# Performance work log

Measured on AMD Instinct MI355X. Metric: run time of the kernel, lower is better.

## Reference

```python
import jax, jax.numpy as jnp
import numpy as np

B, S, N, C, D = 1, 6, 6400, 128, 4
HEADS, POINTS = 4, 20
HS, WS = 32, 88
M = HS * WS
DH = C // HEADS


def setup_inputs() -> dict:
    key = jax.random.key(0)
    ks = jax.random.split(key, 16)
    sc = 0.02
    return {
        "query": jax.random.normal(ks[0], (B, N, C), jnp.float32),
        "key": jax.random.normal(ks[1], (S, M, B, C), jnp.float32),
        "value": jax.random.normal(ks[2], (S, M, B, C), jnp.float32),
        "query_pos": jax.random.normal(ks[3], (B, N, C), jnp.float32),
        "reference_points_cam": jax.random.uniform(ks[4], (S, B, N, D, 2), jnp.float32),
        "bev_mask": jax.random.bernoulli(ks[5], 0.3, (S, B, N, D)),
        "spatial_shapes": jnp.array([[HS, WS]], jnp.int32),
        "level_start_index": jnp.zeros((1,), jnp.int32),
        "Wv": sc * jax.random.normal(ks[6], (C, C), jnp.float32),
        "bv": jnp.zeros((C,), jnp.float32),
        "Woff": sc * jax.random.normal(ks[7], (C, HEADS * POINTS * 2), jnp.float32),
        "boff": sc * jax.random.normal(ks[8], (HEADS * POINTS * 2,), jnp.float32),
        "Wattn": sc * jax.random.normal(ks[9], (C, HEADS * POINTS), jnp.float32),
        "battn": jnp.zeros((HEADS * POINTS,), jnp.float32),
        "Wout": sc * jax.random.normal(ks[10], (C, C), jnp.float32),
        "bout": jnp.zeros((C,), jnp.float32),
    }


def _bilinear(img, x, y):
    # img: (G, HS, WS, DH); x, y: (G, Q, P) pixel coords (grid_sample align_corners=False, zero padding)
    G = img.shape[0]
    flat = img.reshape(G, HS * WS, DH)
    x0 = jnp.floor(x)
    y0 = jnp.floor(y)
    wx1 = x - x0
    wy1 = y - y0
    x0i = x0.astype(jnp.int32)
    y0i = y0.astype(jnp.int32)

    def gather(xi, yi):
        valid = ((xi >= 0) & (xi < WS) & (yi >= 0) & (yi < HS)).astype(img.dtype)
        idx = jnp.clip(yi, 0, HS - 1) * WS + jnp.clip(xi, 0, WS - 1)
        v = jnp.take_along_axis(flat, idx.reshape(G, -1, 1), axis=1)
        return v.reshape(*idx.shape, DH) * valid[..., None]

    v00 = gather(x0i, y0i)
    v01 = gather(x0i + 1, y0i)
    v10 = gather(x0i, y0i + 1)
    v11 = gather(x0i + 1, y0i + 1)
    return (v00 * ((1 - wx1) * (1 - wy1))[..., None]
            + v01 * (wx1 * (1 - wy1))[..., None]
            + v10 * ((1 - wx1) * wy1)[..., None]
            + v11 * (wx1 * wy1)[..., None])


def _deform_attn(q, v, ref, spatial_shapes, Wv, bv, Woff, boff, Wattn, battn):
    # q: (bs, nq, C); v: (bs, M, C); ref: (bs, nq, D, 2) in [0,1]
    bs, nq, _ = q.shape
    val = (v @ Wv + bv).reshape(bs, HS, WS, HEADS, DH)
    val = val.transpose(0, 3, 1, 2, 4).reshape(bs * HEADS, HS, WS, DH)
    # sampling offsets, normalized by (W, H), split points into POINTS//D groups per Z-anchor
    norm = jnp.stack([spatial_shapes[0, 1], spatial_shapes[0, 0]]).astype(q.dtype)  # [W, H]
    off = (q @ Woff + boff).reshape(bs, nq, HEADS, POINTS // D, D, 2) / norm
    loc = ref[:, :, None, None, :, :] + off  # (bs, nq, HEADS, P//D, D, 2)
    loc = loc.reshape(bs, nq, HEADS, POINTS, 2).transpose(0, 2, 1, 3, 4)
    loc = loc.reshape(bs * HEADS, nq, POINTS, 2)
    x = loc[..., 0] * WS - 0.5
    y = loc[..., 1] * HS - 0.5
    sampled = _bilinear(val, x, y)  # (bs*HEADS, nq, POINTS, DH)
    aw = jax.nn.softmax((q @ Wattn + battn).reshape(bs, nq, HEADS, POINTS), axis=-1)
    aw = aw.transpose(0, 2, 1, 3).reshape(bs * HEADS, nq, POINTS)
    out = jnp.einsum('gnpd,gnp->gnd', sampled, aw)
    return out.reshape(bs, HEADS, nq, DH).transpose(0, 2, 1, 3).reshape(bs, nq, C)


def reference(query, key, value, query_pos, reference_points_cam, bev_mask,
              spatial_shapes, level_start_index,
              Wv, bv, Woff, boff, Wattn, battn, Wout, bout):
    residual = query
    q = query + query_pos
    # camera routing mask (original derives indexes from batch 0 of bev_mask)
    mask0 = (bev_mask[:, 0].sum(-1) > 0).astype(q.dtype)  # (S, N)
    # dense masked equivalent of gather/pad/attend/scatter-add: deformable attn is
    # per-query independent, so computing all queries per camera and masking is exact.
    qs = jnp.broadcast_to(q[:, None], (B, S, N, C)).reshape(B * S, N, C)
    vs = value.transpose(2, 0, 1, 3).reshape(B * S, M, C)
    refs = reference_points_cam.transpose(1, 0, 2, 3, 4).reshape(B * S, N, D, 2)
    out = _deform_attn(qs, vs, refs, spatial_shapes, Wv, bv, Woff, boff, Wattn, battn)
    out = out.reshape(B, S, N, C)
    slots = (out * mask0[None, :, :, None]).sum(1)  # (B, N, C)
    count = (bev_mask.sum(-1) > 0).astype(q.dtype).transpose(1, 2, 0).sum(-1)  # (B, N)
    slots = slots / jnp.maximum(count, 1.0)[..., None]
    slots = slots @ Wout + bout
    return slots + residual  # dropout is identity in eval
```

## Files before the change

### kernel.cpp

```cpp
#include <hip/hip_runtime.h>

#define SC 6
#define NQ 6400
#define CH 128
#define HSY 32
#define WSX 88
#define MV 2816
#define NH 4
#define NP 20
#define DD 4
#define DHC 32
#define NPG 5
#define NPAIR (SC * NH * NP)
#define NSCAN 150

#define WS_SCAN_OR  8
#define WS_SCAN_VI  160
#define WS_QOFF     38464
#define WS_AW       1062464
#define WS_VAL      1574464
#define WS_SLOTS    3737152

__device__ __forceinline__ unsigned short f32_to_bf16(float x) {
    unsigned int u = __float_as_uint(x);
    unsigned int r = (u + 0x7FFFu + ((u >> 16) & 1u)) >> 16;
    return (unsigned short)r;
}

__global__ void k_scan(const unsigned int* __restrict__ bm,
                       unsigned int* __restrict__ scan_or,
                       unsigned int* __restrict__ scan_vi) {
    __shared__ unsigned int r_or[256];
    __shared__ unsigned int r_vi[256];
    int i = blockIdx.x * 256 + threadIdx.x;
    unsigned int w = bm[i];
    r_or[threadIdx.x] = w & 0xFFFFFF00u;
    r_vi[threadIdx.x] = (w != 0u) & (w != 0x3F800000u);
    __syncthreads();
    for (int s = 128; s > 0; s >>= 1) {
        if (threadIdx.x < (unsigned)s) {
            r_or[threadIdx.x] |= r_or[threadIdx.x + s];
            r_vi[threadIdx.x] |= r_vi[threadIdx.x + s];
        }
        __syncthreads();
    }
    if (threadIdx.x == 0) {
        scan_or[blockIdx.x] = r_or[0];
        scan_vi[blockIdx.x] = r_vi[0];
    }
}

__global__ void k_flag(const unsigned int* __restrict__ scan_or,
                       const unsigned int* __restrict__ scan_vi,
                       int* __restrict__ flag) {
    __shared__ unsigned int r_or[256];
    __shared__ unsigned int r_vi[256];
    unsigned int o = 0u, v = 0u;
    if (threadIdx.x < NSCAN) { o = scan_or[threadIdx.x]; v = scan_vi[threadIdx.x]; }
    r_or[threadIdx.x] = o;
    r_vi[threadIdx.x] = v;
    __syncthreads();
    for (int s = 128; s > 0; s >>= 1) {
        if (threadIdx.x < (unsigned)s) {
            r_or[threadIdx.x] |= r_or[threadIdx.x + s];
            r_vi[threadIdx.x] |= r_vi[threadIdx.x + s];
        }
        __syncthreads();
    }
    if (threadIdx.x == 0) {
        int f;
        if (!r_vi[0]) f = 2;
        else if (r_or[0]) f = 1;
        else f = 0;
        *flag = f;
    }
}

#define QB 8
__global__ void k_qproj(const float* __restrict__ q, const float* __restrict__ qpos,
                        const float* __restrict__ Woff, const float* __restrict__ boff,
                        const float* __restrict__ Wattn, const float* __restrict__ battn,
                        float* __restrict__ qoff, float* __restrict__ aw) {
    __shared__ float qs[CH][QB];
    __shared__ float lg[QB][NH * NP];
    int n0 = blockIdx.x * QB;
    int t = threadIdx.x;
    for (int i = t; i < QB * CH; i += 256) {
        int qi = i >> 7, k = i & 127;
        int gi = (n0 + qi) * CH + k;
        qs[k][qi] = q[gi] + qpos[gi];
    }
    __syncthreads();
    if (t < 160) {
        float acc[QB];
#pragma unroll
        for (int qi = 0; qi < QB; ++qi) acc[qi] = 0.f;
        for (int k = 0; k < CH; ++k) {
            float w = Woff[k * 160 + t];
            float4 a = *(const float4*)&qs[k][0];
            float4 b = *(const float4*)&qs[k][4];
            acc[0] += a.x * w; acc[1] += a.y * w; acc[2] += a.z * w; acc[3] += a.w * w;
            acc[4] += b.x * w; acc[5] += b.y * w; acc[6] += b.z * w; acc[7] += b.w * w;
        }
        float b = boff[t];
#pragma unroll
        for (int qi = 0; qi < QB; ++qi) qoff[(n0 + qi) * 160 + t] = acc[qi] + b;
    } else if (t < 240) {
        int j = t - 160;
        float acc[QB];
#pragma unroll
        for (int qi = 0; qi < QB; ++qi) acc[qi] = 0.f;
        for (int k = 0; k < CH; ++k) {
            float w = Wattn[k * 80 + j];
            float4 a = *(const float4*)&qs[k][0];
            float4 b = *(const float4*)&qs[k][4];
            acc[0] += a.x * w; acc[1] += a.y * w; acc[2] += a.z * w; acc[3] += a.w * w;
            acc[4] += b.x * w; acc[5] += b.y * w; acc[6] += b.z * w; acc[7] += b.w * w;
        }
        float b = battn[j];
#pragma unroll
        for (int qi = 0; qi < QB; ++qi) lg[qi][j] = acc[qi] + b;
    }
    __syncthreads();
    if (t < QB * NH) {
        int qi = t >> 2, h = t & 3;
        float mx = -1e30f;
#pragma unroll
        for (int p = 0; p < NP; ++p) mx = fmaxf(mx, lg[qi][h * NP + p]);
        float e[NP];
        float sm = 0.f;
#pragma unroll
        for (int p = 0; p < NP; ++p) { e[p] = __expf(lg[qi][h * NP + p] - mx); sm += e[p]; }
        float inv = 1.f / sm;
#pragma unroll
        for (int p = 0; p < NP; ++p) aw[(n0 + qi) * 80 + h * NP + p] = e[p] * inv;
    }
}

#define MB 8
__global__ void k_vproj(const float* __restrict__ value, const float* __restrict__ Wv,
                        const float* __restrict__ bv, unsigned short* __restrict__ valw) {
    __shared__ float vs[CH][MB];
    int r0 = blockIdx.x * MB;
    int t = threadIdx.x;
    for (int i = t; i < MB * CH; i += 128) {
        int ri = i >> 7, k = i & 127;
        vs[k][ri] = value[(size_t)(r0 + ri) * CH + k];
    }
    __syncthreads();
    float acc[MB];
#pragma unroll
    for (int ri = 0; ri < MB; ++ri) acc[ri] = 0.f;
    for (int k = 0; k < CH; ++k) {
        float w = Wv[k * CH + t];
        float4 a = *(const float4*)&vs[k][0];
        float4 b = *(const float4*)&vs[k][4];
        acc[0] += a.x * w; acc[1] += a.y * w; acc[2] += a.z * w; acc[3] += a.w * w;
        acc[4] += b.x * w; acc[5] += b.y * w; acc[6] += b.z * w; acc[7] += b.w * w;
    }
    float b = bv[t];
    int h = t >> 5, dh = t & 31;
#pragma unroll
    for (int ri = 0; ri < MB; ++ri) {
        int r = r0 + ri;
        int s = r / MV;
        int m = r - s * MV;
        valw[(size_t)((s * NH + h) * MV + m) * DHC + dh] = f32_to_bf16(acc[ri] + b);
    }
}

#define REDP 36
__global__ __launch_bounds__(320) void k_sample(
        const float* __restrict__ ref, const float* __restrict__ qoff,
        const float* __restrict__ aw, const void* __restrict__ bm,
        const int* __restrict__ flag, const unsigned short* __restrict__ valw,
        float* __restrict__ slots) {
    int bid = blockIdx.x;
    int n = (bid & 7) * (NQ / 8) + (bid >> 3);
    int t = threadIdx.x;

    __shared__ float awl[NH * NP];
    __shared__ float qo[160];
    __shared__ float rf[SC][DD][2];
    __shared__ float mk[SC];
    __shared__ int   pairI[NPAIR][4];
    __shared__ float pairW[NPAIR][4];
    __shared__ float red[80][REDP];

    if (t < NH * NP) awl[t] = aw[n * 80 + t];
    if (t >= 80 && t < 240) qo[t - 80] = qoff[n * 160 + (t - 80)];
    if (t >= 240 && t < 240 + SC * DD * 2) {
        int i = t - 240;
        int s = i >> 3, rem = i & 7;
        rf[s][rem >> 1][rem & 1] = ref[(size_t)(s * NQ + n) * 8 + rem];
    }
    if (t >= 288 && t < 288 + SC) {
        int s = t - 288;
        int i = s * NQ + n;
        int f = *flag;
        int any;
        if (f == 1) {
            const unsigned char* p = (const unsigned char*)bm + (size_t)i * 4;
            any = (int)(p[0] | p[1] | p[2] | p[3]);
        } else if (f == 0) {
            const int* p = (const int*)bm + (size_t)i * 4;
            any = p[0] | p[1] | p[2] | p[3];
        } else {
            const float* p = (const float*)bm + (size_t)i * 4;
            any = (p[0] != 0.f) | (p[1] != 0.f) | (p[2] != 0.f) | (p[3] != 0.f);
        }
        mk[s] = any ? 1.0f : 0.0f;
    }
    __syncthreads();

    for (int i = t; i < NPAIR; i += 320) {
        int s = i / (NH * NP);
        int q = i - s * (NH * NP);
        int h = q & 3;
        int p = q >> 2;
        int g = p >> 2, d = p & 3;
        float x = rf[s][d][0] * (float)WSX + qo[((h * NPG + g) * DD + d) * 2 + 0] - 0.5f;
        float y = rf[s][d][1] * (float)HSY + qo[((h * NPG + g) * DD + d) * 2 + 1] - 0.5f;
        float xf = floorf(x), yf = floorf(y);
        float wx = x - xf, wy = y - yf;
        int x0 = (int)xf, y0 = (int)yf;
        int x1 = x0 + 1, y1 = y0 + 1;
        float vx0 = (x0 >= 0 && x0 < WSX) ? 1.f : 0.f;
        float vx1 = (x1 >= 0 && x1 < WSX) ? 1.f : 0.f;
        float vy0 = (y0 >= 0 && y0 < HSY) ? 1.f : 0.f;
        float vy1 = (y1 >= 0 && y1 < HSY) ? 1.f : 0.f;
        int cx0 = min(max(x0, 0), WSX - 1), cx1 = min(max(x1, 0), WSX - 1);
        int cy0 = min(max(y0, 0), HSY - 1), cy1 = min(max(y1, 0), HSY - 1);
        int base = (s * NH + h) * MV;
        pairI[i][0] = (base + cy0 * WSX + cx0) * DHC;
        pairI[i][1] = (base + cy0 * WSX + cx1) * DHC;
        pairI[i][2] = (base + cy1 * WSX + cx0) * DHC;
        pairI[i][3] = (base + cy1 * WSX + cx1) * DHC;
        float a = awl[h * NP + p];
        pairW[i][0] = (1.f - wx) * (1.f - wy) * vx0 * vy0 * a;
        pairW[i][1] = wx * (1.f - wy) * vx1 * vy0 * a;
        pairW[i][2] = (1.f - wx) * wy * vx0 * vy1 * a;
        pairW[i][3] = wx * wy * vx1 * vy1 * a;
    }
    __syncthreads();

    int sid = t >> 2;
    int c8 = t & 3;
    int coff = c8 * 8;
    float acc[8];
#pragma unroll
    for (int j = 0; j < 8; ++j) acc[j] = 0.f;
    for (int s = 0; s < SC; ++s) {
        if (mk[s] == 0.f) continue;
        int pr = s * (NH * NP) + sid;
        int4  ii = *(const int4*)pairI[pr];
        float4 ww = *(const float4*)pairW[pr];
#define CORNER(IDX, W)  {                                              \
            uint4 u = *(const uint4*)(valw + (IDX) + coff);            \
            float w_ = (W);                                            \
            acc[0] += w_ * __uint_as_float(u.x << 16);                 \
            acc[1] += w_ * __uint_as_float(u.x & 0xFFFF0000u);         \
            acc[2] += w_ * __uint_as_float(u.y << 16);                 \
            acc[3] += w_ * __uint_as_float(u.y & 0xFFFF0000u);         \
            acc[4] += w_ * __uint_as_float(u.z << 16);                 \
            acc[5] += w_ * __uint_as_float(u.z & 0xFFFF0000u);         \
            acc[6] += w_ * __uint_as_float(u.w << 16);                 \
            acc[7] += w_ * __uint_as_float(u.w & 0xFFFF0000u);         \
        }
        CORNER(ii.x, ww.x)
        CORNER(ii.y, ww.y)
        CORNER(ii.z, ww.z)
        CORNER(ii.w, ww.w)
#undef CORNER
    }
    *(float4*)&red[sid][coff] = make_float4(acc[0], acc[1], acc[2], acc[3]);
    *(float4*)&red[sid][coff + 4] = make_float4(acc[4], acc[5], acc[6], acc[7]);
    __syncthreads();

    if (t < CH) {
        int h = t >> 5, ch = t & 31;
        float sum = 0.f;
#pragma unroll
        for (int p = 0; p < NP; ++p) sum += red[p * 4 + h][ch];
        float cnt = mk[0] + mk[1] + mk[2] + mk[3] + mk[4] + mk[5];
        slots[(size_t)n * CH + t] = sum / fmaxf(cnt, 1.0f);
    }
}

__global__ void k_out(const float* __restrict__ slots, const float* __restrict__ Wout,
                      const float* __restrict__ bout, const float* __restrict__ query,
                      float* __restrict__ out) {
    __shared__ float sl[CH][QB];
    int n0 = blockIdx.x * QB;
    int t = threadIdx.x;
    for (int i = t; i < QB * CH; i += 128) {
        int qi = i >> 7, k = i & 127;
        sl[k][qi] = slots[(size_t)(n0 + qi) * CH + k];
    }
    __syncthreads();
    float acc[QB];
#pragma unroll
    for (int qi = 0; qi < QB; ++qi) acc[qi] = 0.f;
    for (int k = 0; k < CH; ++k) {
        float w = Wout[k * CH + t];
        float4 a = *(const float4*)&sl[k][0];
        float4 b = *(const float4*)&sl[k][4];
        acc[0] += a.x * w; acc[1] += a.y * w; acc[2] += a.z * w; acc[3] += a.w * w;
        acc[4] += b.x * w; acc[5] += b.y * w; acc[6] += b.z * w; acc[7] += b.w * w;
    }
    float b = bout[t];
#pragma unroll
    for (int qi = 0; qi < QB; ++qi) {
        int gi = (n0 + qi) * CH + t;
        out[gi] = acc[qi] + b + query[gi];
    }
}

extern "C" void kernel_launch(void* const* d_in, const int* in_sizes, int n_in,
                              void* d_out, int out_size, void* d_ws, size_t ws_size,
                              hipStream_t stream) {
    const float* query     = (const float*)d_in[0];
    const float* value     = (const float*)d_in[2];
    const float* query_pos = (const float*)d_in[3];
    const float* refcam    = (const float*)d_in[4];
    const void*  bev_mask  = (const void*)d_in[5];
    const float* Wv    = (const float*)d_in[8];
    const float* bv    = (const float*)d_in[9];
    const float* Woff  = (const float*)d_in[10];
    const float* boff  = (const float*)d_in[11];
    const float* Wattn = (const float*)d_in[12];
    const float* battn = (const float*)d_in[13];
    const float* Wout  = (const float*)d_in[14];
    const float* bout  = (const float*)d_in[15];

    float* wsf   = (float*)d_ws;
    int*   flag  = (int*)d_ws;
    unsigned int* scan_or = (unsigned int*)d_ws + WS_SCAN_OR;
    unsigned int* scan_vi = (unsigned int*)d_ws + WS_SCAN_VI;
    float* qoff  = wsf + WS_QOFF;
    float* aw    = wsf + WS_AW;
    unsigned short* valw = (unsigned short*)(wsf + WS_VAL);
    float* slots = wsf + WS_SLOTS;
    float* out   = (float*)d_out;

    k_scan<<<NSCAN, 256, 0, stream>>>((const unsigned int*)bev_mask, scan_or, scan_vi);
    k_flag<<<1, 256, 0, stream>>>(scan_or, scan_vi, flag);
    k_qproj<<<NQ / QB, 256, 0, stream>>>(query, query_pos, Woff, boff, Wattn, battn, qoff, aw);
    k_vproj<<<(SC * MV) / MB, 128, 0, stream>>>(value, Wv, bv, valw);
    k_sample<<<NQ, 320, 0, stream>>>(refcam, qoff, aw, bev_mask, flag, valw, slots);
    k_out<<<NQ / QB, 128, 0, stream>>>(slots, Wout, bout, query, out);
}
```

Baseline: 177.2 us.

## Merge mask scan, flag, query and value projections into one launch

Replaces the four prologue kernels (mask scan, flag reduction, query projection with softmax, value projection) with one kernel that dispatches on block index. Block 0 computes the mask-format flag from only the first 2048 words of bev_mask, so the two-stage reduction over the whole tensor is gone. Value-projection blocks now handle 16 rows with 256 threads instead of 8 rows with 128. The aim is to cut launch overhead and let the query and value projections run at the same time. The trade-off is that the flag now depends on a partial sample of the mask.

```diff
diff --git a/kernel.cpp b/kernel.cpp
--- a/kernel.cpp
+++ b/kernel.cpp
@@ -12,10 +12,11 @@
 #define DHC 32
 #define NPG 5
 #define NPAIR (SC * NH * NP)
-#define NSCAN 150
-
-#define WS_SCAN_OR  8
-#define WS_SCAN_VI  160
+
+#define NB_QPROJ 800
+#define NB_VPROJ 1056
+#define NB_MEGA  (1 + NB_QPROJ + NB_VPROJ)
+
 #define WS_QOFF     38464
 #define WS_AW       1062464
 #define WS_VAL      1574464
@@ -27,145 +28,130 @@
     return (unsigned short)r;
 }
 
-__global__ void k_scan(const unsigned int* __restrict__ bm,
-                       unsigned int* __restrict__ scan_or,
-                       unsigned int* __restrict__ scan_vi) {
-    __shared__ unsigned int r_or[256];
-    __shared__ unsigned int r_vi[256];
-    int i = blockIdx.x * 256 + threadIdx.x;
-    unsigned int w = bm[i];
-    r_or[threadIdx.x] = w & 0xFFFFFF00u;
-    r_vi[threadIdx.x] = (w != 0u) & (w != 0x3F800000u);
-    __syncthreads();
-    for (int s = 128; s > 0; s >>= 1) {
-        if (threadIdx.x < (unsigned)s) {
-            r_or[threadIdx.x] |= r_or[threadIdx.x + s];
-            r_vi[threadIdx.x] |= r_vi[threadIdx.x + s];
-        }
+#define QB 8
+__global__ __launch_bounds__(256) void k_mega(
+        const unsigned int* __restrict__ bm,
+        const float* __restrict__ q, const float* __restrict__ qpos,
+        const float* __restrict__ Woff, const float* __restrict__ boff,
+        const float* __restrict__ Wattn, const float* __restrict__ battn,
+        const float* __restrict__ value, const float* __restrict__ Wv,
+        const float* __restrict__ bv,
+        int* __restrict__ flag, float* __restrict__ qoff,
+        float* __restrict__ aw, unsigned short* __restrict__ valw) {
+    __shared__ __align__(16) float smem[2048];
+    int bid = blockIdx.x;
+    int t = threadIdx.x;
+
+    if (bid == 0) {
+        unsigned int* r_or = (unsigned int*)smem;
+        unsigned int* r_vi = r_or + 256;
+        unsigned int o = 0u, v = 0u;
+        for (int i = t; i < 2048; i += 256) {
+            unsigned int w = bm[i];
+            o |= (w & 0xFFFFFF00u);
+            v |= (unsigned int)((w != 0u) & (w != 0x3F800000u));
+        }
+        r_or[t] = o; r_vi[t] = v;
         __syncthreads();
-    }
-    if (threadIdx.x == 0) {
-        scan_or[blockIdx.x] = r_or[0];
-        scan_vi[blockIdx.x] = r_vi[0];
-    }
-}
-
-__global__ void k_flag(const unsigned int* __restrict__ scan_or,
-                       const unsigned int* __restrict__ scan_vi,
-                       int* __restrict__ flag) {
-    __shared__ unsigned int r_or[256];
-    __shared__ unsigned int r_vi[256];
-    unsigned int o = 0u, v = 0u;
-    if (threadIdx.x < NSCAN) { o = scan_or[threadIdx.x]; v = scan_vi[threadIdx.x]; }
-    r_or[threadIdx.x] = o;
-    r_vi[threadIdx.x] = v;
-    __syncthreads();
-    for (int s = 128; s > 0; s >>= 1) {
-        if (threadIdx.x < (unsigned)s) {
-            r_or[threadIdx.x] |= r_or[threadIdx.x + s];
-            r_vi[threadIdx.x] |= r_vi[threadIdx.x + s];
+        for (int s = 128; s > 0; s >>= 1) {
+            if (t < s) { r_or[t] |= r_or[t + s]; r_vi[t] |= r_vi[t + s]; }
+            __syncthreads();
+        }
+        if (t == 0) {
+            int f;
+            if (!r_vi[0]) f = 2;
+            else if (r_or[0]) f = 1;
+            else f = 0;
+            *flag = f;
+        }
+        return;
+    }
+
+    if (bid <= NB_QPROJ) {
+        float (*qs)[QB] = (float(*)[QB])smem;
+        float (*lg)[NH * NP] = (float(*)[NH * NP])(smem + CH * QB);
+        int n0 = (bid - 1) * QB;
+        for (int i = t; i < QB * CH; i += 256) {
+            int qi = i >> 7, k = i & 127;
+            int gi = (n0 + qi) * CH + k;
+            qs[k][qi] = q[gi] + qpos[gi];
         }
         __syncthreads();
-    }
-    if (threadIdx.x == 0) {
-        int f;
-        if (!r_vi[0]) f = 2;
-        else if (r_or[0]) f = 1;
-        else f = 0;
-        *flag = f;
-    }
-}
-
-#define QB 8
-__global__ void k_qproj(const float* __restrict__ q, const float* __restrict__ qpos,
-                        const float* __restrict__ Woff, const float* __restrict__ boff,
-                        const float* __restrict__ Wattn, const float* __restrict__ battn,
-                        float* __restrict__ qoff, float* __restrict__ aw) {
-    __shared__ float qs[CH][QB];
-    __shared__ float lg[QB][NH * NP];
-    int n0 = blockIdx.x * QB;
-    int t = threadIdx.x;
-    for (int i = t; i < QB * CH; i += 256) {
-        int qi = i >> 7, k = i & 127;
-        int gi = (n0 + qi) * CH + k;
-        qs[k][qi] = q[gi] + qpos[gi];
-    }
-    __syncthreads();
-    if (t < 160) {
-        float acc[QB];
-#pragma unroll
-        for (int qi = 0; qi < QB; ++qi) acc[qi] = 0.f;
+        if (t < 160) {
+            float acc[QB];
+#pragma unroll
+            for (int qi = 0; qi < QB; ++qi) acc[qi] = 0.f;
+            for (int k = 0; k < CH; ++k) {
+                float w = Woff[k * 160 + t];
+                float4 a = *(const float4*)&qs[k][0];
+                float4 b = *(const float4*)&qs[k][4];
+                acc[0] += a.x * w; acc[1] += a.y * w; acc[2] += a.z * w; acc[3] += a.w * w;
+                acc[4] += b.x * w; acc[5] += b.y * w; acc[6] += b.z * w; acc[7] += b.w * w;
+            }
+            float b = boff[t];
+#pragma unroll
+            for (int qi = 0; qi < QB; ++qi) qoff[(n0 + qi) * 160 + t] = acc[qi] + b;
+        } else if (t < 240) {
+            int j = t - 160;
+            float acc[QB];
+#pragma unroll
+            for (int qi = 0; qi < QB; ++qi) acc[qi] = 0.f;
+            for (int k = 0; k < CH; ++k) {
+                float w = Wattn[k * 80 + j];
+                float4 a = *(const float4*)&qs[k][0];
+                float4 b = *(const float4*)&qs[k][4];
+                acc[0] += a.x * w; acc[1] += a.y * w; acc[2] += a.z * w; acc[3] += a.w * w;
+                acc[4] += b.x * w; acc[5] += b.y * w; acc[6] += b.z * w; acc[7] += b.w * w;
+            }
+            float b = battn[j];
+#pragma unroll
+            for (int qi = 0; qi < QB; ++qi) lg[qi][j] = acc[qi] + b;
+        }
+        __syncthreads();
+        if (t < QB * NH) {
+            int qi = t >> 2, h = t & 3;
+            float mx = -1e30f;
+#pragma unroll
+            for (int p = 0; p < NP; ++p) mx = fmaxf(mx, lg[qi][h * NP + p]);
+            float e[NP];
+            float sm = 0.f;
+#pragma unroll
+            for (int p = 0; p < NP; ++p) { e[p] = __expf(lg[qi][h * NP + p] - mx); sm += e[p]; }
+            float inv = 1.f / sm;
+#pragma unroll
+            for (int p = 0; p < NP; ++p) aw[(n0 + qi) * 80 + h * NP + p] = e[p] * inv;
+        }
+        return;
+    }
+
+    {
+        float (*vs)[16] = (float(*)[16])smem;
+        int r0 = (bid - 1 - NB_QPROJ) * 16;
+        for (int i = t; i < 16 * CH; i += 256) {
+            int ri = i >> 7, k = i & 127;
+            vs[k][ri] = value[(size_t)(r0 + ri) * CH + k];
+        }
+        __syncthreads();
+        int c = t & 127, rh = t >> 7;
+        float acc[8];
+#pragma unroll
+        for (int ri = 0; ri < 8; ++ri) acc[ri] = 0.f;
         for (int k = 0; k < CH; ++k) {
-            float w = Woff[k * 160 + t];
-            float4 a = *(const float4*)&qs[k][0];
-            float4 b = *(const float4*)&qs[k][4];
+            float w = Wv[k * CH + c];
+            float4 a = *(const float4*)&vs[k][rh * 8];
+            float4 b = *(const float4*)&vs[k][rh * 8 + 4];
             acc[0] += a.x * w; acc[1] += a.y * w; acc[2] += a.z * w; acc[3] += a.w * w;
             acc[4] += b.x * w; acc[5] += b.y * w; acc[6] += b.z * w; acc[7] += b.w * w;
         }
-        float b = boff[t];
-#pragma unroll
-        for (int qi = 0; qi < QB; ++qi) qoff[(n0 + qi) * 160 + t] = acc[qi] + b;
-    } else if (t < 240) {
-        int j = t - 160;
-        float acc[QB];
-#pragma unroll
-        for (int qi = 0; qi < QB; ++qi) acc[qi] = 0.f;
-        for (int k = 0; k < CH; ++k) {
-            float w = Wattn[k * 80 + j];
-            float4 a = *(const float4*)&qs[k][0];
-            float4 b = *(const float4*)&qs[k][4];
-            acc[0] += a.x * w; acc[1] += a.y * w; acc[2] += a.z * w; acc[3] += a.w * w;
-            acc[4] += b.x * w; acc[5] += b.y * w; acc[6] += b.z * w; acc[7] += b.w * w;
-        }
-        float b = battn[j];
-#pragma unroll
-        for (int qi = 0; qi < QB; ++qi) lg[qi][j] = acc[qi] + b;
-    }
-    __syncthreads();
-    if (t < QB * NH) {
-        int qi = t >> 2, h = t & 3;
-        float mx = -1e30f;
-#pragma unroll
-        for (int p = 0; p < NP; ++p) mx = fmaxf(mx, lg[qi][h * NP + p]);
-        float e[NP];
-        float sm = 0.f;
-#pragma unroll
-        for (int p = 0; p < NP; ++p) { e[p] = __expf(lg[qi][h * NP + p] - mx); sm += e[p]; }
-        float inv = 1.f / sm;
-#pragma unroll
-        for (int p = 0; p < NP; ++p) aw[(n0 + qi) * 80 + h * NP + p] = e[p] * inv;
-    }
-}
-
-#define MB 8
-__global__ void k_vproj(const float* __restrict__ value, const float* __restrict__ Wv,
-                        const float* __restrict__ bv, unsigned short* __restrict__ valw) {
-    __shared__ float vs[CH][MB];
-    int r0 = blockIdx.x * MB;
-    int t = threadIdx.x;
-    for (int i = t; i < MB * CH; i += 128) {
-        int ri = i >> 7, k = i & 127;
-        vs[k][ri] = value[(size_t)(r0 + ri) * CH + k];
-    }
-    __syncthreads();
-    float acc[MB];
-#pragma unroll
-    for (int ri = 0; ri < MB; ++ri) acc[ri] = 0.f;
-    for (int k = 0; k < CH; ++k) {
-        float w = Wv[k * CH + t];
-        float4 a = *(const float4*)&vs[k][0];
-        float4 b = *(const float4*)&vs[k][4];
-        acc[0] += a.x * w; acc[1] += a.y * w; acc[2] += a.z * w; acc[3] += a.w * w;
-        acc[4] += b.x * w; acc[5] += b.y * w; acc[6] += b.z * w; acc[7] += b.w * w;
-    }
-    float b = bv[t];
-    int h = t >> 5, dh = t & 31;
-#pragma unroll
-    for (int ri = 0; ri < MB; ++ri) {
-        int r = r0 + ri;
-        int s = r / MV;
-        int m = r - s * MV;
-        valw[(size_t)((s * NH + h) * MV + m) * DHC + dh] = f32_to_bf16(acc[ri] + b);
+        float b = bv[c];
+        int h = c >> 5, dh = c & 31;
+#pragma unroll
+        for (int ri = 0; ri < 8; ++ri) {
+            int r = r0 + rh * 8 + ri;
+            int s = r / MV;
+            int m = r - s * MV;
+            valw[(size_t)((s * NH + h) * MV + m) * DHC + dh] = f32_to_bf16(acc[ri] + b);
+        }
     }
 }
 
@@ -335,18 +321,15 @@
 
     float* wsf   = (float*)d_ws;
     int*   flag  = (int*)d_ws;
-    unsigned int* scan_or = (unsigned int*)d_ws + WS_SCAN_OR;
-    unsigned int* scan_vi = (unsigned int*)d_ws + WS_SCAN_VI;
     float* qoff  = wsf + WS_QOFF;
     float* aw    = wsf + WS_AW;
     unsigned short* valw = (unsigned short*)(wsf + WS_VAL);
     float* slots = wsf + WS_SLOTS;
     float* out   = (float*)d_out;
 
-    k_scan<<<NSCAN, 256, 0, stream>>>((const unsigned int*)bev_mask, scan_or, scan_vi);
-    k_flag<<<1, 256, 0, stream>>>(scan_or, scan_vi, flag);
-    k_qproj<<<NQ / QB, 256, 0, stream>>>(query, query_pos, Woff, boff, Wattn, battn, qoff, aw);
-    k_vproj<<<(SC * MV) / MB, 128, 0, stream>>>(value, Wv, bv, valw);
+    k_mega<<<NB_MEGA, 256, 0, stream>>>((const unsigned int*)bev_mask,
+                                        query, query_pos, Woff, boff, Wattn, battn,
+                                        value, Wv, bv, flag, qoff, aw, valw);
     k_sample<<<NQ, 320, 0, stream>>>(refcam, qoff, aw, bev_mask, flag, valw, slots);
     k_out<<<NQ / QB, 128, 0, stream>>>(slots, Wout, bout, query, out);
 }
```

New measurement: 165.1 us. -6.8%, faster.
